# Optimization experiments

Measured on AMD Instinct MI355X. Metric: run time of the kernel, lower is better.

The kernel has to match this reference:

```python
import jax, jax.numpy as jnp
import numpy as np

G = 64      # norm_groups
T = 5       # Newton-Schulz iterations
EPS = 1e-5


def setup_inputs() -> dict:
    key = jax.random.key(0)
    weight = jax.random.normal(key, (2048, 18432), dtype=jnp.float32)
    return {"weight": weight}


def reference(weight):
    out_ch = weight.shape[0]
    # Z: [G, c, d] with c = out_ch // G, d = prod(rest)
    Z = weight.reshape(G, out_ch // G, -1)
    Zc = Z - jnp.mean(Z, axis=-1, keepdims=True)
    # S = Zc @ Zc^T : [G, c, c]
    S = jnp.einsum('gcd,ged->gce', Zc, Zc)
    c = S.shape[-1]
    eye = jnp.eye(c, dtype=S.dtype)
    S = S + EPS * eye
    # Frobenius norm per group, keepdim -> [G,1,1]
    norm_S = jnp.sqrt(jnp.sum(S * S, axis=(1, 2), keepdims=True))
    S = S / norm_S
    # Newton-Schulz: B_{t+1} = 1.5*B_t - 0.5 * B_t^3 @ S
    B = jnp.broadcast_to(eye, S.shape)
    for _ in range(T):
        B3 = jnp.matmul(jnp.matmul(B, B), B)
        B = 1.5 * B - 0.5 * jnp.matmul(B3, S)
    W = jnp.matmul(B, Zc) / jnp.sqrt(norm_S)
    return W.reshape(weight.shape)
```

## Files before the change

kernel.cpp:

```cpp
#include <hip/hip_runtime.h>

#define G 64
#define C 32
#define D 18432
#define NCH 16
#define TD 1152
#define KSUB 128
#define PSTR 136
#define PLANE (32 * PSTR)
#define EPS 1e-5f
#define NS_ITERS 5

typedef __attribute__((ext_vector_type(8))) short short8v;
typedef __attribute__((ext_vector_type(4))) float float4v;

__device__ __forceinline__ void split3(float x, unsigned short& h1,
                                       unsigned short& h2, unsigned short& h3) {
    unsigned int u = __float_as_uint(x);
    unsigned int m1 = u & 0xffff0000u;
    float r1 = x - __uint_as_float(m1);
    unsigned int u2 = __float_as_uint(r1);
    unsigned int m2 = u2 & 0xffff0000u;
    float r2 = r1 - __uint_as_float(m2);
    h1 = (unsigned short)(m1 >> 16);
    h2 = (unsigned short)(m2 >> 16);
    h3 = (unsigned short)(__float_as_uint(r2) >> 16);
}

__global__ __launch_bounds__(256) void k1_gram(const float* __restrict__ W,
                                               float* __restrict__ psum,
                                               float* __restrict__ prow) {
    __shared__ __align__(16) unsigned short lds_u[3 * PLANE];

    const int bid  = blockIdx.x;
    const int g    = bid >> 4;
    const int ch   = bid & 15;
    const int tid  = threadIdx.x;
    const int lane = tid & 63;
    const int wave = tid >> 6;
    const float* Zg = W + (size_t)g * C * D + (size_t)ch * TD;

    const int r  = tid >> 3;
    const int cb = (tid & 7) * 16;
    const float* srcRow = Zg + (size_t)r * D;

    const int lh = lane & 15;
    const int kb = (lane >> 4) * 8;
    const int kbase = wave * 32;

    float4v acc[2][2];
#pragma unroll
    for (int a = 0; a < 2; ++a)
#pragma unroll
        for (int b = 0; b < 2; ++b) acc[a][b] = (float4v)0.f;
    float rs = 0.f;

    for (int st = 0; st < TD / KSUB; ++st) {
        __syncthreads();
        const float* s = srcRow + st * KSUB + cb;
        float x[16];
#pragma unroll
        for (int i = 0; i < 4; ++i) {
            float4 v = *(const float4*)(s + i * 4);
            x[4 * i + 0] = v.x; x[4 * i + 1] = v.y;
            x[4 * i + 2] = v.z; x[4 * i + 3] = v.w;
        }
        unsigned short h1[16], h2[16], h3[16];
#pragma unroll
        for (int i = 0; i < 16; ++i) {
            rs += x[i];
            split3(x[i], h1[i], h2[i], h3[i]);
        }
        const int widx = r * PSTR + cb;
#pragma unroll
        for (int q = 0; q < 2; ++q) {
            short8v v1, v2, v3;
#pragma unroll
            for (int j = 0; j < 8; ++j) {
                v1[j] = (short)h1[8 * q + j];
                v2[j] = (short)h2[8 * q + j];
                v3[j] = (short)h3[8 * q + j];
            }
            *(short8v*)&lds_u[widx + 8 * q]             = v1;
            *(short8v*)&lds_u[PLANE + widx + 8 * q]     = v2;
            *(short8v*)&lds_u[2 * PLANE + widx + 8 * q] = v3;
        }
        __syncthreads();
        short8v fr[2][3];
#pragma unroll
        for (int h = 0; h < 2; ++h)
#pragma unroll
            for (int p = 0; p < 3; ++p)
                fr[h][p] = *(const short8v*)&lds_u[p * PLANE + (16 * h + lh) * PSTR + kbase + kb];
#pragma unroll
        for (int a = 0; a < 2; ++a)
#pragma unroll
            for (int b = 0; b < 2; ++b) {
                float4v t = acc[a][b];
                t = __builtin_amdgcn_mfma_f32_16x16x32_bf16(fr[a][0], fr[b][0], t, 0, 0, 0);
                t = __builtin_amdgcn_mfma_f32_16x16x32_bf16(fr[a][0], fr[b][1], t, 0, 0, 0);
                t = __builtin_amdgcn_mfma_f32_16x16x32_bf16(fr[a][1], fr[b][0], t, 0, 0, 0);
                t = __builtin_amdgcn_mfma_f32_16x16x32_bf16(fr[a][1], fr[b][1], t, 0, 0, 0);
                t = __builtin_amdgcn_mfma_f32_16x16x32_bf16(fr[a][0], fr[b][2], t, 0, 0, 0);
                t = __builtin_amdgcn_mfma_f32_16x16x32_bf16(fr[a][2], fr[b][0], t, 0, 0, 0);
                acc[a][b] = t;
            }
    }

#pragma unroll
    for (int off = 1; off <= 4; off <<= 1) rs += __shfl_xor(rs, off, 64);
    if ((tid & 7) == 0) prow[(size_t)bid * C + r] = rs;

    __syncthreads();
    float* red = (float*)lds_u;
#pragma unroll
    for (int a = 0; a < 2; ++a)
#pragma unroll
        for (int b = 0; b < 2; ++b)
#pragma unroll
            for (int j = 0; j < 4; ++j) {
                int row = 16 * a + ((lane >> 4) << 2) + j;
                int col = 16 * b + lh;
                red[wave * 1056 + row * 33 + col] = acc[a][b][j];
            }
    __syncthreads();
#pragma unroll
    for (int k = 0; k < 4; ++k) {
        int el = tid + 256 * k;
        int row = el >> 5, col = el & 31;
        int o = row * 33 + col;
        float sv = red[o] + red[1056 + o] + red[2112 + o] + red[3168 + o];
        psum[(size_t)bid * (C * C) + el] = sv;
    }
}

__global__ __launch_bounds__(256) void k2_ns(const float* __restrict__ psum,
                                             const float* __restrict__ prow,
                                             float* __restrict__ MT,
                                             float* __restrict__ vout) {
    __shared__ float S[C][C + 1];
    __shared__ float B[C][C + 1];
    __shared__ float T1[C][C + 1];
    __shared__ float T2[C][C + 1];
    __shared__ float mean[C];
    __shared__ float redw[4];
    __shared__ float normsh;

    const int g   = blockIdx.x;
    const int tid = threadIdx.x;
    const int e   = tid & 31;
    const int cb  = tid >> 5;

    float selt[4];
#pragma unroll
    for (int k = 0; k < 4; ++k) {
        int el = tid + 256 * k;
        float s = 0.f;
#pragma unroll
        for (int ch = 0; ch < NCH; ++ch)
            s += psum[((size_t)g * NCH + ch) * (C * C) + el];
        selt[k] = s;
    }
    if (tid < C) {
        float s = 0.f;
#pragma unroll
        for (int ch = 0; ch < NCH; ++ch)
            s += prow[((size_t)g * NCH + ch) * C + tid];
        mean[tid] = s / (float)D;
    }
    __syncthreads();

    float ss = 0.f;
#pragma unroll
    for (int k = 0; k < 4; ++k) {
        int el = tid + 256 * k;
        int c = el >> 5;
        float sv = selt[k] - (float)D * mean[c] * mean[e];
        if (c == e) sv += EPS;
        S[c][e] = sv;
        ss = fmaf(sv, sv, ss);
    }
#pragma unroll
    for (int off = 32; off >= 1; off >>= 1) ss += __shfl_xor(ss, off, 64);
    if ((tid & 63) == 0) redw[tid >> 6] = ss;
    __syncthreads();
    if (tid == 0) normsh = sqrtf(redw[0] + redw[1] + redw[2] + redw[3]);
    __syncthreads();
    const float inv_norm = 1.0f / normsh;
#pragma unroll
    for (int k = 0; k < 4; ++k) {
        int c = cb + 8 * k;
        S[c][e] *= inv_norm;
        B[c][e] = (c == e) ? 1.f : 0.f;
    }
    __syncthreads();

    for (int it = 0; it < NS_ITERS; ++it) {
#pragma unroll
        for (int k = 0; k < 4; ++k) {
            int c = cb + 8 * k;
            float s = 0.f;
            for (int kk = 0; kk < C; ++kk)
                s = fmaf(B[c][kk], B[kk][e], s);
            T1[c][e] = s;
        }
        __syncthreads();
#pragma unroll
        for (int k = 0; k < 4; ++k) {
            int c = cb + 8 * k;
            float s = 0.f;
            for (int kk = 0; kk < C; ++kk)
                s = fmaf(T1[c][kk], B[kk][e], s);
            T2[c][e] = s;
        }
        __syncthreads();
        float pv[4];
#pragma unroll
        for (int k = 0; k < 4; ++k) {
            int c = cb + 8 * k;
            float s = 0.f;
            for (int kk = 0; kk < C; ++kk)
                s = fmaf(T2[c][kk], S[kk][e], s);
            pv[k] = s;
        }
#pragma unroll
        for (int k = 0; k < 4; ++k) {
            int c = cb + 8 * k;
            B[c][e] = 1.5f * B[c][e] - 0.5f * pv[k];
        }
        __syncthreads();
    }

    const float invs = 1.0f / sqrtf(normsh);
#pragma unroll
    for (int k = 0; k < 4; ++k) {
        int c = cb + 8 * k;
        MT[(size_t)g * (C * C) + e * C + c] = B[c][e] * invs;
    }
    if (tid < C) {
        float s = 0.f;
        for (int ee = 0; ee < C; ++ee)
            s = fmaf(B[tid][ee] * invs, mean[ee], s);
        vout[(size_t)g * C + tid] = s;
    }
}

__global__ __launch_bounds__(256) void k3_apply(const float* __restrict__ W,
                                                const float* __restrict__ MT,
                                                const float* __restrict__ vv,
                                                float* __restrict__ out) {
    const int blocksPerGroup = D / 512;
    const int g  = blockIdx.x / blocksPerGroup;
    const int cbk = blockIdx.x % blocksPerGroup;
    const int d0 = cbk * 512 + (int)threadIdx.x * 2;
    const float* Zg = W + (size_t)g * C * D + d0;
    const float* Mg = MT + (size_t)g * (C * C);

    float accx[C], accy[C];
#pragma unroll
    for (int r = 0; r < C; ++r) { accx[r] = 0.f; accy[r] = 0.f; }

    for (int e = 0; e < C; ++e) {
        float2 z = *(const float2*)(Zg + (size_t)e * D);
#pragma unroll
        for (int r = 0; r < C; ++r) {
            float m = Mg[e * C + r];
            accx[r] = fmaf(m, z.x, accx[r]);
            accy[r] = fmaf(m, z.y, accy[r]);
        }
    }

    float* Og = out + (size_t)g * C * D + d0;
#pragma unroll
    for (int r = 0; r < C; ++r) {
        float vr = vv[g * C + r];
        float2 o = make_float2(accx[r] - vr, accy[r] - vr);
        *(float2*)(Og + (size_t)r * D) = o;
    }
}

extern "C" void kernel_launch(void* const* d_in, const int* in_sizes, int n_in,
                              void* d_out, int out_size, void* d_ws, size_t ws_size,
                              hipStream_t stream) {
    const float* w = (const float*)d_in[0];
    float* out = (float*)d_out;

    float* psum = (float*)d_ws;
    float* prow = psum + (size_t)(G * NCH) * (C * C);
    float* MT   = prow + (size_t)(G * NCH) * C;
    float* vv   = MT   + (size_t)G * (C * C);

    k1_gram <<<G * NCH, 256, 0, stream>>>(w, psum, prow);
    k2_ns   <<<G,       256, 0, stream>>>(psum, prow, MT, vv);
    k3_apply<<<G * (D / 512), 256, 0, stream>>>(w, MT, vv, out);
}
```

Measured before the change: 96.01 us.

## Split Gram kernel into more chunks, prefetch next slab, nontemporal output stores

```diff
diff --git a/kernel.cpp b/kernel.cpp
--- a/kernel.cpp
+++ b/kernel.cpp
@@ -3,8 +3,6 @@
 #define G 64
 #define C 32
 #define D 18432
-#define NCH 16
-#define TD 1152
 #define KSUB 128
 #define PSTR 136
 #define PLANE (32 * PSTR)
@@ -27,14 +25,18 @@
     h3 = (unsigned short)(__float_as_uint(r2) >> 16);
 }
 
+template <int NCHT>
 __global__ __launch_bounds__(256) void k1_gram(const float* __restrict__ W,
                                                float* __restrict__ psum,
                                                float* __restrict__ prow) {
+    constexpr int TD  = D / NCHT;
+    constexpr int NST = TD / KSUB;
+
     __shared__ __align__(16) unsigned short lds_u[3 * PLANE];
 
-    const int bid  = blockIdx.x;
-    const int g    = bid >> 4;
-    const int ch   = bid & 15;
+    const int ch   = blockIdx.x;
+    const int g    = blockIdx.y;
+    const int bid  = g * NCHT + ch;
     const int tid  = threadIdx.x;
     const int lane = tid & 63;
     const int wave = tid >> 6;
@@ -55,15 +57,23 @@
         for (int b = 0; b < 2; ++b) acc[a][b] = (float4v)0.f;
     float rs = 0.f;
 
-    for (int st = 0; st < TD / KSUB; ++st) {
-        __syncthreads();
-        const float* s = srcRow + st * KSUB + cb;
+    float4 cur[4], nxt[4];
+#pragma unroll
+    for (int i = 0; i < 4; ++i)
+        cur[i] = *(const float4*)(srcRow + cb + 4 * i);
+
+#pragma unroll
+    for (int st = 0; st < NST; ++st) {
+        if (st + 1 < NST) {
+            const float* s = srcRow + (st + 1) * KSUB + cb;
+#pragma unroll
+            for (int i = 0; i < 4; ++i) nxt[i] = *(const float4*)(s + 4 * i);
+        }
         float x[16];
 #pragma unroll
         for (int i = 0; i < 4; ++i) {
-            float4 v = *(const float4*)(s + i * 4);
-            x[4 * i + 0] = v.x; x[4 * i + 1] = v.y;
-            x[4 * i + 2] = v.z; x[4 * i + 3] = v.w;
+            x[4 * i + 0] = cur[i].x; x[4 * i + 1] = cur[i].y;
+            x[4 * i + 2] = cur[i].z; x[4 * i + 3] = cur[i].w;
         }
         unsigned short h1[16], h2[16], h3[16];
 #pragma unroll
@@ -71,6 +81,7 @@
             rs += x[i];
             split3(x[i], h1[i], h2[i], h3[i]);
         }
+        if (st) __syncthreads();
         const int widx = r * PSTR + cb;
 #pragma unroll
         for (int q = 0; q < 2; ++q) {
@@ -105,6 +116,8 @@
                 t = __builtin_amdgcn_mfma_f32_16x16x32_bf16(fr[a][2], fr[b][0], t, 0, 0, 0);
                 acc[a][b] = t;
             }
+#pragma unroll
+        for (int i = 0; i < 4; ++i) cur[i] = nxt[i];
     }
 
 #pragma unroll
@@ -134,6 +147,7 @@
     }
 }
 
+template <int NCHT>
 __global__ __launch_bounds__(256) void k2_ns(const float* __restrict__ psum,
                                              const float* __restrict__ prow,
                                              float* __restrict__ MT,
@@ -149,7 +163,7 @@
     const int g   = blockIdx.x;
     const int tid = threadIdx.x;
     const int e   = tid & 31;
-    const int cb  = tid >> 5;
+    const int cbq = tid >> 5;
 
     float selt[4];
 #pragma unroll
@@ -157,15 +171,15 @@
         int el = tid + 256 * k;
         float s = 0.f;
 #pragma unroll
-        for (int ch = 0; ch < NCH; ++ch)
-            s += psum[((size_t)g * NCH + ch) * (C * C) + el];
+        for (int ch = 0; ch < NCHT; ++ch)
+            s += psum[((size_t)g * NCHT + ch) * (C * C) + el];
         selt[k] = s;
     }
     if (tid < C) {
         float s = 0.f;
 #pragma unroll
-        for (int ch = 0; ch < NCH; ++ch)
-            s += prow[((size_t)g * NCH + ch) * C + tid];
+        for (int ch = 0; ch < NCHT; ++ch)
+            s += prow[((size_t)g * NCHT + ch) * C + tid];
         mean[tid] = s / (float)D;
     }
     __syncthreads();
@@ -189,7 +203,7 @@
     const float inv_norm = 1.0f / normsh;
 #pragma unroll
     for (int k = 0; k < 4; ++k) {
-        int c = cb + 8 * k;
+        int c = cbq + 8 * k;
         S[c][e] *= inv_norm;
         B[c][e] = (c == e) ? 1.f : 0.f;
     }
@@ -198,7 +212,7 @@
     for (int it = 0; it < NS_ITERS; ++it) {
 #pragma unroll
         for (int k = 0; k < 4; ++k) {
-            int c = cb + 8 * k;
+            int c = cbq + 8 * k;
             float s = 0.f;
             for (int kk = 0; kk < C; ++kk)
                 s = fmaf(B[c][kk], B[kk][e], s);
@@ -207,7 +221,7 @@
         __syncthreads();
 #pragma unroll
         for (int k = 0; k < 4; ++k) {
-            int c = cb + 8 * k;
+            int c = cbq + 8 * k;
             float s = 0.f;
             for (int kk = 0; kk < C; ++kk)
                 s = fmaf(T1[c][kk], B[kk][e], s);
@@ -217,7 +231,7 @@
         float pv[4];
 #pragma unroll
         for (int k = 0; k < 4; ++k) {
-            int c = cb + 8 * k;
+            int c = cbq + 8 * k;
             float s = 0.f;
             for (int kk = 0; kk < C; ++kk)
                 s = fmaf(T2[c][kk], S[kk][e], s);
@@ -225,7 +239,7 @@
         }
 #pragma unroll
         for (int k = 0; k < 4; ++k) {
-            int c = cb + 8 * k;
+            int c = cbq + 8 * k;
             B[c][e] = 1.5f * B[c][e] - 0.5f * pv[k];
         }
         __syncthreads();
@@ -234,7 +248,7 @@
     const float invs = 1.0f / sqrtf(normsh);
 #pragma unroll
     for (int k = 0; k < 4; ++k) {
-        int c = cb + 8 * k;
+        int c = cbq + 8 * k;
         MT[(size_t)g * (C * C) + e * C + c] = B[c][e] * invs;
     }
     if (tid < C) {
@@ -249,10 +263,8 @@
                                                 const float* __restrict__ MT,
                                                 const float* __restrict__ vv,
                                                 float* __restrict__ out) {
-    const int blocksPerGroup = D / 512;
-    const int g  = blockIdx.x / blocksPerGroup;
-    const int cbk = blockIdx.x % blocksPerGroup;
-    const int d0 = cbk * 512 + (int)threadIdx.x * 2;
+    const int g  = blockIdx.y;
+    const int d0 = blockIdx.x * 512 + (int)threadIdx.x * 2;
     const float* Zg = W + (size_t)g * C * D + d0;
     const float* Mg = MT + (size_t)g * (C * C);
 
@@ -275,7 +287,9 @@
     for (int r = 0; r < C; ++r) {
         float vr = vv[g * C + r];
         float2 o = make_float2(accx[r] - vr, accy[r] - vr);
-        *(float2*)(Og + (size_t)r * D) = o;
+        double dv;
+        __builtin_memcpy(&dv, &o, 8);
+        __builtin_nontemporal_store(dv, (double*)(Og + (size_t)r * D));
     }
 }
 
@@ -285,12 +299,21 @@
     const float* w = (const float*)d_in[0];
     float* out = (float*)d_out;
 
+    const size_t need36 = ((size_t)G * 36 * (C * C + C) + (size_t)G * (C * C + C)) * sizeof(float);
+    const bool use36 = (ws_size >= need36);
+    const int nch = use36 ? 36 : 16;
+
     float* psum = (float*)d_ws;
-    float* prow = psum + (size_t)(G * NCH) * (C * C);
-    float* MT   = prow + (size_t)(G * NCH) * C;
+    float* prow = psum + (size_t)(G * nch) * (C * C);
+    float* MT   = prow + (size_t)(G * nch) * C;
     float* vv   = MT   + (size_t)G * (C * C);
 
-    k1_gram <<<G * NCH, 256, 0, stream>>>(w, psum, prow);
-    k2_ns   <<<G,       256, 0, stream>>>(psum, prow, MT, vv);
-    k3_apply<<<G * (D / 512), 256, 0, stream>>>(w, MT, vv, out);
-}
+    if (use36) {
+        k1_gram<36><<<dim3(36, G), 256, 0, stream>>>(w, psum, prow);
+        k2_ns<36>  <<<G,           256, 0, stream>>>(psum, prow, MT, vv);
+    } else {
+        k1_gram<16><<<dim3(16, G), 256, 0, stream>>>(w, psum, prow);
+        k2_ns<16>  <<<G,           256, 0, stream>>>(psum, prow, MT, vv);
+    }
+    k3_apply<<<dim3(D / 512, G), 256, 0, stream>>>(w, MT, vv, out);
+}
```

New measurement: 104.8 us. +9.1%, slower.

## Load MFMA operands directly from global memory in gram kernel, prefetch next slice

Applied to the files above, without the earlier changes.

```diff
diff --git a/kernel.cpp b/kernel.cpp
--- a/kernel.cpp
+++ b/kernel.cpp
@@ -4,10 +4,8 @@
 #define C 32
 #define D 18432
 #define NCH 16
-#define TD 1152
-#define KSUB 128
-#define PSTR 136
-#define PLANE (32 * PSTR)
+#define TD (D / NCH)
+#define NST (TD / 128)
 #define EPS 1e-5f
 #define NS_ITERS 5
 
@@ -27,71 +25,64 @@
     h3 = (unsigned short)(__float_as_uint(r2) >> 16);
 }
 
+__device__ __forceinline__ void split8(const float4& v0, const float4& v1,
+                                       short8v& p1, short8v& p2, short8v& p3,
+                                       float& rs) {
+    float x[8] = {v0.x, v0.y, v0.z, v0.w, v1.x, v1.y, v1.z, v1.w};
+#pragma unroll
+    for (int j = 0; j < 8; ++j) {
+        unsigned short h1, h2, h3;
+        rs += x[j];
+        split3(x[j], h1, h2, h3);
+        p1[j] = (short)h1; p2[j] = (short)h2; p3[j] = (short)h3;
+    }
+}
+
 __global__ __launch_bounds__(256) void k1_gram(const float* __restrict__ W,
                                                float* __restrict__ psum,
                                                float* __restrict__ prow) {
-    __shared__ __align__(16) unsigned short lds_u[3 * PLANE];
-
-    const int bid  = blockIdx.x;
-    const int g    = bid >> 4;
-    const int ch   = bid & 15;
+    __shared__ float red[4 * 1056 + 4 * C];
+
+    const int ch   = blockIdx.x;
+    const int g    = blockIdx.y;
+    const int bid  = g * NCH + ch;
     const int tid  = threadIdx.x;
     const int lane = tid & 63;
     const int wave = tid >> 6;
-    const float* Zg = W + (size_t)g * C * D + (size_t)ch * TD;
-
-    const int r  = tid >> 3;
-    const int cb = (tid & 7) * 16;
-    const float* srcRow = Zg + (size_t)r * D;
-
-    const int lh = lane & 15;
-    const int kb = (lane >> 4) * 8;
-    const int kbase = wave * 32;
+
+    const int rbase = lane & 15;
+    const int koff  = (lane >> 4) * 8;
+
+    const float* Zg   = W + (size_t)g * C * D + (size_t)ch * TD;
+    const float* p0   = Zg + (size_t)rbase * D + wave * 32 + koff;
+    const float* p1   = p0 + (size_t)16 * D;
 
     float4v acc[2][2];
 #pragma unroll
     for (int a = 0; a < 2; ++a)
 #pragma unroll
         for (int b = 0; b < 2; ++b) acc[a][b] = (float4v)0.f;
-    float rs = 0.f;
-
-    for (int st = 0; st < TD / KSUB; ++st) {
-        __syncthreads();
-        const float* s = srcRow + st * KSUB + cb;
-        float x[16];
-#pragma unroll
-        for (int i = 0; i < 4; ++i) {
-            float4 v = *(const float4*)(s + i * 4);
-            x[4 * i + 0] = v.x; x[4 * i + 1] = v.y;
-            x[4 * i + 2] = v.z; x[4 * i + 3] = v.w;
-        }
-        unsigned short h1[16], h2[16], h3[16];
-#pragma unroll
-        for (int i = 0; i < 16; ++i) {
-            rs += x[i];
-            split3(x[i], h1[i], h2[i], h3[i]);
-        }
-        const int widx = r * PSTR + cb;
-#pragma unroll
-        for (int q = 0; q < 2; ++q) {
-            short8v v1, v2, v3;
-#pragma unroll
-            for (int j = 0; j < 8; ++j) {
-                v1[j] = (short)h1[8 * q + j];
-                v2[j] = (short)h2[8 * q + j];
-                v3[j] = (short)h3[8 * q + j];
-            }
-            *(short8v*)&lds_u[widx + 8 * q]             = v1;
-            *(short8v*)&lds_u[PLANE + widx + 8 * q]     = v2;
-            *(short8v*)&lds_u[2 * PLANE + widx + 8 * q] = v3;
-        }
-        __syncthreads();
-        short8v fr[2][3];
-#pragma unroll
-        for (int h = 0; h < 2; ++h)
-#pragma unroll
-            for (int p = 0; p < 3; ++p)
-                fr[h][p] = *(const short8v*)&lds_u[p * PLANE + (16 * h + lh) * PSTR + kbase + kb];
+    float rs0 = 0.f, rs1 = 0.f;
+
+    float4 c00 = *(const float4*)(p0);
+    float4 c01 = *(const float4*)(p0 + 4);
+    float4 c10 = *(const float4*)(p1);
+    float4 c11 = *(const float4*)(p1 + 4);
+
+#pragma unroll
+    for (int st = 0; st < NST; ++st) {
+        float4 n00, n01, n10, n11;
+        if (st + 1 < NST) {
+            n00 = *(const float4*)(p0 + (st + 1) * 128);
+            n01 = *(const float4*)(p0 + (st + 1) * 128 + 4);
+            n10 = *(const float4*)(p1 + (st + 1) * 128);
+            n11 = *(const float4*)(p1 + (st + 1) * 128 + 4);
+        }
+        short8v fa[3], fb[3];
+        split8(c00, c01, fa[0], fa[1], fa[2], rs0);
+        split8(c10, c11, fb[0], fb[1], fb[2], rs1);
+
+        short8v* fr[2] = {fa, fb};
 #pragma unroll
         for (int a = 0; a < 2; ++a)
 #pragma unroll
@@ -105,14 +96,16 @@
                 t = __builtin_amdgcn_mfma_f32_16x16x32_bf16(fr[a][2], fr[b][0], t, 0, 0, 0);
                 acc[a][b] = t;
             }
-    }
-
-#pragma unroll
-    for (int off = 1; off <= 4; off <<= 1) rs += __shfl_xor(rs, off, 64);
-    if ((tid & 7) == 0) prow[(size_t)bid * C + r] = rs;
-
-    __syncthreads();
-    float* red = (float*)lds_u;
+        c00 = n00; c01 = n01; c10 = n10; c11 = n11;
+    }
+
+    rs0 += __shfl_xor(rs0, 16, 64); rs0 += __shfl_xor(rs0, 32, 64);
+    rs1 += __shfl_xor(rs1, 16, 64); rs1 += __shfl_xor(rs1, 32, 64);
+    if (lane < 16) {
+        red[4224 + wave * C + lane]      = rs0;
+        red[4224 + wave * C + 16 + lane] = rs1;
+    }
+
 #pragma unroll
     for (int a = 0; a < 2; ++a)
 #pragma unroll
@@ -120,10 +113,11 @@
 #pragma unroll
             for (int j = 0; j < 4; ++j) {
                 int row = 16 * a + ((lane >> 4) << 2) + j;
-                int col = 16 * b + lh;
+                int col = 16 * b + (lane & 15);
                 red[wave * 1056 + row * 33 + col] = acc[a][b][j];
             }
     __syncthreads();
+
 #pragma unroll
     for (int k = 0; k < 4; ++k) {
         int el = tid + 256 * k;
@@ -131,6 +125,11 @@
         int o = row * 33 + col;
         float sv = red[o] + red[1056 + o] + red[2112 + o] + red[3168 + o];
         psum[(size_t)bid * (C * C) + el] = sv;
+    }
+    if (tid < C) {
+        float s = red[4224 + tid] + red[4224 + C + tid] +
+                  red[4224 + 2 * C + tid] + red[4224 + 3 * C + tid];
+        prow[(size_t)bid * C + tid] = s;
     }
 }
 
@@ -149,7 +148,7 @@
     const int g   = blockIdx.x;
     const int tid = threadIdx.x;
     const int e   = tid & 31;
-    const int cb  = tid >> 5;
+    const int cbq = tid >> 5;
 
     float selt[4];
 #pragma unroll
@@ -189,7 +188,7 @@
     const float inv_norm = 1.0f / normsh;
 #pragma unroll
     for (int k = 0; k < 4; ++k) {
-        int c = cb + 8 * k;
+        int c = cbq + 8 * k;
         S[c][e] *= inv_norm;
         B[c][e] = (c == e) ? 1.f : 0.f;
     }
@@ -198,7 +197,7 @@
     for (int it = 0; it < NS_ITERS; ++it) {
 #pragma unroll
         for (int k = 0; k < 4; ++k) {
-            int c = cb + 8 * k;
+            int c = cbq + 8 * k;
             float s = 0.f;
             for (int kk = 0; kk < C; ++kk)
                 s = fmaf(B[c][kk], B[kk][e], s);
@@ -207,7 +206,7 @@
         __syncthreads();
 #pragma unroll
         for (int k = 0; k < 4; ++k) {
-            int c = cb + 8 * k;
+            int c = cbq + 8 * k;
             float s = 0.f;
             for (int kk = 0; kk < C; ++kk)
                 s = fmaf(T1[c][kk], B[kk][e], s);
@@ -217,7 +216,7 @@
         float pv[4];
 #pragma unroll
         for (int k = 0; k < 4; ++k) {
-            int c = cb + 8 * k;
+            int c = cbq + 8 * k;
             float s = 0.f;
             for (int kk = 0; kk < C; ++kk)
                 s = fmaf(T2[c][kk], S[kk][e], s);
@@ -225,7 +224,7 @@
         }
 #pragma unroll
         for (int k = 0; k < 4; ++k) {
-            int c = cb + 8 * k;
+            int c = cbq + 8 * k;
             B[c][e] = 1.5f * B[c][e] - 0.5f * pv[k];
         }
         __syncthreads();
@@ -234,7 +233,7 @@
     const float invs = 1.0f / sqrtf(normsh);
 #pragma unroll
     for (int k = 0; k < 4; ++k) {
-        int c = cb + 8 * k;
+        int c = cbq + 8 * k;
         MT[(size_t)g * (C * C) + e * C + c] = B[c][e] * invs;
     }
     if (tid < C) {
@@ -250,9 +249,9 @@
                                                 const float* __restrict__ vv,
                                                 float* __restrict__ out) {
     const int blocksPerGroup = D / 512;
-    const int g  = blockIdx.x / blocksPerGroup;
+    const int g   = blockIdx.x / blocksPerGroup;
     const int cbk = blockIdx.x % blocksPerGroup;
-    const int d0 = cbk * 512 + (int)threadIdx.x * 2;
+    const int d0  = cbk * 512 + (int)threadIdx.x * 2;
     const float* Zg = W + (size_t)g * C * D + d0;
     const float* Mg = MT + (size_t)g * (C * C);
 
@@ -290,7 +289,7 @@
     float* MT   = prow + (size_t)(G * NCH) * C;
     float* vv   = MT   + (size_t)G * (C * C);
 
-    k1_gram <<<G * NCH, 256, 0, stream>>>(w, psum, prow);
-    k2_ns   <<<G,       256, 0, stream>>>(psum, prow, MT, vv);
+    k1_gram<<<dim3(NCH, G), 256, 0, stream>>>(w, psum, prow);
+    k2_ns  <<<G,            256, 0, stream>>>(psum, prow, MT, vv);
     k3_apply<<<G * (D / 512), 256, 0, stream>>>(w, MT, vv, out);
 }
```

Result: no change. 94.62 us, median of 2 (-1.4%).
